# Performance work log

Measured on AMD Instinct MI355X. Metric: run time of the kernel, lower is better.

Reference implementation:

```python
import jax, jax.numpy as jnp
import numpy as np

E, TOPK, H, F, CAP, TP = 8, 2, 1024, 4096, 2048, 1
N = 8192  # tokens * topk (token copies)


def setup_inputs() -> dict:
    key = jax.random.key(0)
    ks = jax.random.split(key, 6)
    inputs_shard = jax.random.normal(ks[0], (N, H), jnp.float32)
    gate_weight = jax.random.uniform(ks[1], (N,), jnp.float32)
    choosed_experts = jax.random.randint(ks[2], (N,), 0, E, dtype=jnp.int32)
    new_index = jax.random.permutation(ks[3], N).astype(jnp.int32)
    w1 = jax.random.normal(ks[4], (E, F, H), jnp.float32) * 0.02
    w2 = jax.random.normal(ks[5], (E, H, F), jnp.float32) * 0.02
    return {"inputs_shard": inputs_shard, "gate_weight": gate_weight,
            "choosed_experts": choosed_experts, "new_index": new_index,
            "w1": w1, "w2": w2}


def _grouped_expert_mlp(x, experts, w1, w2):
    # capacity-based grouped GEMM: sort token copies by expert, pack into
    # (E, CAP, H), run batched fc1->gelu->fc2, unpack back to token order.
    n = x.shape[0]
    order = jnp.argsort(experts)                      # [N]
    se = experts[order]
    offsets = jnp.searchsorted(se, jnp.arange(E))     # start of each expert block
    rank = jnp.arange(n) - offsets[se]                # within-expert position
    valid = rank < CAP                                # CAP=2*N/E, ~never drops
    slot = jnp.where(valid, se * CAP + rank, E * CAP) # out-of-range -> dropped
    buf = jnp.zeros((E * CAP, x.shape[1]), x.dtype).at[slot].set(x[order], mode="drop")
    xe = buf.reshape(E, CAP, -1)                      # [E, CAP, H]
    h = jax.nn.gelu(jnp.einsum("ech,efh->ecf", xe, w1), approximate=False)
    ye = jnp.einsum("ecf,ehf->ech", h, w2).reshape(E * CAP, -1)
    y_sorted = jnp.where(valid[:, None], ye[jnp.clip(slot, 0, E * CAP - 1)], 0.0)
    return jnp.zeros_like(x).at[order].set(y_sorted)  # back to token-copy order


def reference(inputs_shard, gate_weight, choosed_experts, new_index, w1, w2):
    # expert compute, scaled by router probabilities (combine-side scaling)
    result = _grouped_expert_mlp(inputs_shard, choosed_experts, w1, w2)
    result = result * gate_weight[:, None]
    # scatter combine: output1[new_index] = result; full_output += output1
    full_output = jnp.zeros((N, H), result.dtype).at[new_index].set(result)
    # topk reduce: view(N//topk, topk, H).sum(1)
    topk_reduce = full_output.reshape(N // TOPK, TOPK, H).sum(1)
    # reduce_scatter over TP group; TP=1 => identity
    return topk_reduce
```

## Files before the change

kernel.cpp:

```cpp
#include <hip/hip_runtime.h>
#include <stdint.h>

#define N_TOK 8192
#define HDIM  1024
#define FDIM  4096
#define NEXP  8
#define MAXTILES 72
#define CVTZ  8
#define CVT1B 2048

typedef __attribute__((ext_vector_type(8))) __bf16 bf16x8;
typedef __attribute__((ext_vector_type(8))) unsigned short ushort8v;
typedef __attribute__((ext_vector_type(4))) unsigned short ushort4v;
typedef __attribute__((ext_vector_type(4))) float floatx4;

__device__ __forceinline__ unsigned short f2bf(float f) {
  union { float f; uint32_t u; } v; v.f = f;
  uint32_t u = v.u;
  return (unsigned short)((u + 0x7FFFu + ((u >> 16) & 1u)) >> 16);
}

__device__ __forceinline__ void load_lds16(const void* g, void* l) {
  __builtin_amdgcn_global_load_lds(
      (const __attribute__((address_space(1))) void*)(uintptr_t)g,
      (__attribute__((address_space(3))) void*)(uint32_t)(uintptr_t)l,
      16, 0, 0);
}


__global__ void k_count(const int* __restrict__ experts, int* __restrict__ meta) {
  int i = blockIdx.x * 256 + threadIdx.x;
  atomicAdd(&meta[experts[i]], 1);
}

__global__ void k_plan(int* __restrict__ meta) {
  if (threadIdx.x == 0) {
    int off = 0, nt = 0;
    for (int e = 0; e < NEXP; ++e) {
      int c = meta[e];
      meta[8 + e] = off;
      meta[16 + e] = off;
      int t = (c + 127) >> 7;
      for (int k = 0; k < t; ++k) meta[32 + nt++] = (e << 16) | k;
      off += c;
    }
    meta[24] = nt;
  }
}

__global__ void k_scatterpack(const float* __restrict__ x, const int* __restrict__ experts,
                              int* __restrict__ meta, int* __restrict__ order,
                              unsigned short* __restrict__ xs,
                              const float* __restrict__ w1, unsigned short* __restrict__ w1b) {
  int b = blockIdx.x;
  int t = threadIdx.x;
  if (b < N_TOK) {
    __shared__ int spos;
    if (t == 0) {
      int e = experts[b];
      int pos = atomicAdd(&meta[16 + e], 1);
      order[pos] = b;
      spos = pos;
    }
    __syncthreads();
    int s = spos;
    float4 v = *(const float4*)(x + (size_t)b * HDIM + t * 4);
    ushort4v u;
    u[0] = f2bf(v.x); u[1] = f2bf(v.y); u[2] = f2bf(v.z); u[3] = f2bf(v.w);
    *(ushort4v*)(xs + (size_t)s * HDIM + t * 4) = u;
  } else {
    int cb = b - N_TOK;
    const int per = (int)((size_t)NEXP * FDIM * HDIM / 4 / CVT1B);
    size_t base = (size_t)cb * per;
    for (int j = t; j < per; j += 256) {
      size_t idx = (base + j) * 4;
      float4 v = *(const float4*)(w1 + idx);
      ushort4v u;
      u[0] = f2bf(v.x); u[1] = f2bf(v.y); u[2] = f2bf(v.z); u[3] = f2bf(v.w);
      *(ushort4v*)(w1b + idx) = u;
    }
  }
}

template <bool PRE>
__global__ __launch_bounds__(256) void gemm1_t(
    const unsigned short* __restrict__ xs, const void* __restrict__ w1v,
    unsigned short* __restrict__ h1, const int* __restrict__ meta,
    const float* __restrict__ w2src, unsigned short* __restrict__ w2dst) {
  if constexpr (PRE) {
    if (blockIdx.z < CVTZ) {
      int cvtid = blockIdx.z * gridDim.x + blockIdx.x;
      const int per = (int)((size_t)NEXP * HDIM * FDIM / 4 / (CVTZ * (FDIM / 128)));
      size_t base = (size_t)cvtid * per;
      for (int j = threadIdx.x; j < per; j += 256) {
        size_t idx = (base + j) * 4;
        float4 v = *(const float4*)(w2src + idx);
        ushort4v u;
        u[0] = f2bf(v.x); u[1] = f2bf(v.y); u[2] = f2bf(v.z); u[3] = f2bf(v.w);
        *(ushort4v*)(w2dst + idx) = u;
      }
      return;
    }
  }
  __shared__ unsigned short As[2 * 128 * 32];
  __shared__ unsigned short Bs[2 * 128 * 32];

  int bx = blockIdx.z - (PRE ? CVTZ : 0);
  if (bx >= meta[24]) return;
  int entry = meta[32 + bx];
  int e = entry >> 16, mt = entry & 0xffff;
  int row0 = meta[8 + e] + mt * 128;
  int rend = meta[8 + e] + meta[e];
  int fBase = blockIdx.x * 128;

  int tid = threadIdx.x;
  int w = tid >> 6, lane = tid & 63;
  int r = lane & 15, q = lane >> 4;
  int wm = (w >> 1) * 64, wn = (w & 1) * 64;

  int ar0 = (w * 16) + (lane >> 2);
  int s0 = min(row0 + ar0, N_TOK - 1);
  int s1 = min(row0 + 64 + ar0, N_TOK - 1);
  const unsigned short* ag0 = xs + (size_t)s0 * HDIM + (lane & 3) * 8;
  const unsigned short* ag1 = xs + (size_t)s1 * HDIM + (lane & 3) * 8;
  unsigned short* al0 = &As[(w * 16) * 32];
  unsigned short* al1 = &As[(64 + w * 16) * 32];

  const unsigned short* bg0 = nullptr; const unsigned short* bg1 = nullptr;
  unsigned short* bl0 = nullptr; unsigned short* bl1 = nullptr;
  const float* wbase = nullptr; int brow = 0, bkk = 0;
  if constexpr (PRE) {
    const unsigned short* wb = (const unsigned short*)w1v;
    int br = w * 16 + (lane >> 2);
    bg0 = wb + ((size_t)e * FDIM + fBase + br) * HDIM + (lane & 3) * 8;
    bg1 = bg0 + (size_t)64 * HDIM;
    bl0 = &Bs[(w * 16) * 32];
    bl1 = &Bs[(64 + w * 16) * 32];
  } else {
    brow = tid >> 1; bkk = (tid & 1) * 16;
    wbase = (const float*)w1v + ((size_t)e * FDIM + fBase + brow) * HDIM + bkk;
  }

  auto stage = [&](int kk, int bo) {
    load_lds16(ag0 + kk, al0 + bo);
    load_lds16(ag1 + kk, al1 + bo);
    if constexpr (PRE) {
      load_lds16(bg0 + kk, bl0 + bo);
      load_lds16(bg1 + kk, bl1 + bo);
    } else {
      const float* gb = wbase + kk;
      float4 f0 = *(const float4*)(gb);
      float4 f1 = *(const float4*)(gb + 4);
      float4 f2 = *(const float4*)(gb + 8);
      float4 f3 = *(const float4*)(gb + 12);
      ushort8v u0, u1;
      u0[0] = f2bf(f0.x); u0[1] = f2bf(f0.y); u0[2] = f2bf(f0.z); u0[3] = f2bf(f0.w);
      u0[4] = f2bf(f1.x); u0[5] = f2bf(f1.y); u0[6] = f2bf(f1.z); u0[7] = f2bf(f1.w);
      u1[0] = f2bf(f2.x); u1[1] = f2bf(f2.y); u1[2] = f2bf(f2.z); u1[3] = f2bf(f2.w);
      u1[4] = f2bf(f3.x); u1[5] = f2bf(f3.y); u1[6] = f2bf(f3.z); u1[7] = f2bf(f3.w);
      *(ushort8v*)&Bs[bo + brow * 32 + bkk] = u0;
      *(ushort8v*)&Bs[bo + brow * 32 + bkk + 8] = u1;
    }
  };

  floatx4 acc[4][4];
#pragma unroll
  for (int i = 0; i < 4; ++i)
#pragma unroll
    for (int j = 0; j < 4; ++j) acc[i][j] = (floatx4){0.f, 0.f, 0.f, 0.f};

  stage(0, 0);
  for (int k0 = 0; k0 < HDIM; k0 += 32) {
    int bo = ((k0 >> 5) & 1) * 4096;
    __syncthreads();
    if (k0 + 32 < HDIM) stage(k0 + 32, bo ^ 4096);

    bf16x8 av[4], bv[4];
#pragma unroll
    for (int i = 0; i < 4; ++i)
      av[i] = __builtin_bit_cast(bf16x8, *(const ushort8v*)&As[bo + (wm + i * 16 + r) * 32 + q * 8]);
#pragma unroll
    for (int j = 0; j < 4; ++j)
      bv[j] = __builtin_bit_cast(bf16x8, *(const ushort8v*)&Bs[bo + (wn + j * 16 + r) * 32 + q * 8]);
#pragma unroll
    for (int i = 0; i < 4; ++i)
#pragma unroll
      for (int j = 0; j < 4; ++j)
        acc[i][j] = __builtin_amdgcn_mfma_f32_16x16x32_bf16(av[i], bv[j], acc[i][j], 0, 0, 0);
  }

#pragma unroll
  for (int i = 0; i < 4; ++i) {
    int mrow = row0 + wm + i * 16 + q * 4;
#pragma unroll
    for (int reg = 0; reg < 4; ++reg) {
      int s = mrow + reg;
      if (s < rend) {
        unsigned short* dst = h1 + (size_t)s * FDIM + fBase + wn + r;
#pragma unroll
        for (int j = 0; j < 4; ++j) {
          float v = acc[i][j][reg];
          float g = 0.5f * v * (1.0f + erff(v * 0.70710678118654752f));
          dst[j * 16] = f2bf(g);
        }
      }
    }
  }
}

template <bool PRE>
__global__ __launch_bounds__(256) void gemm2_t(
    const unsigned short* __restrict__ h1, const void* __restrict__ w2v,
    const float* __restrict__ gate, const int* __restrict__ new_index,
    float* __restrict__ out, const int* __restrict__ meta) {
  __shared__ unsigned short As[2 * 128 * 32];
  __shared__ unsigned short Bs[2 * 128 * 32];

  int bx = blockIdx.z;
  if (bx >= meta[24]) return;
  int entry = meta[32 + bx];
  int e = entry >> 16, mt = entry & 0xffff;
  int row0 = meta[8 + e] + mt * 128;
  int rend = meta[8 + e] + meta[e];
  int nBase = blockIdx.x * 128;
  int kStart = blockIdx.y * (FDIM / 2);
  int kEnd = kStart + (FDIM / 2);
  const int* order = meta + 256;

  int tid = threadIdx.x;
  int w = tid >> 6, lane = tid & 63;
  int r = lane & 15, q = lane >> 4;
  int wm = (w >> 1) * 64, wn = (w & 1) * 64;

  int ar0 = (w * 16) + (lane >> 2);
  int s0 = min(row0 + ar0, N_TOK - 1);
  int s1 = min(row0 + 64 + ar0, N_TOK - 1);
  const unsigned short* ag0 = h1 + (size_t)s0 * FDIM + (lane & 3) * 8;
  const unsigned short* ag1 = h1 + (size_t)s1 * FDIM + (lane & 3) * 8;
  unsigned short* al0 = &As[(w * 16) * 32];
  unsigned short* al1 = &As[(64 + w * 16) * 32];

  const unsigned short* bg0 = nullptr; const unsigned short* bg1 = nullptr;
  unsigned short* bl0 = nullptr; unsigned short* bl1 = nullptr;
  const float* wbase = nullptr; int brow = 0, bkk = 0;
  if constexpr (PRE) {
    const unsigned short* wb = (const unsigned short*)w2v;
    int br = w * 16 + (lane >> 2);
    bg0 = wb + ((size_t)e * HDIM + nBase + br) * FDIM + (lane & 3) * 8;
    bg1 = bg0 + (size_t)64 * FDIM;
    bl0 = &Bs[(w * 16) * 32];
    bl1 = &Bs[(64 + w * 16) * 32];
  } else {
    brow = tid >> 1; bkk = (tid & 1) * 16;
    wbase = (const float*)w2v + ((size_t)e * HDIM + nBase + brow) * FDIM + bkk;
  }

  auto stage = [&](int kk, int bo) {
    load_lds16(ag0 + kk, al0 + bo);
    load_lds16(ag1 + kk, al1 + bo);
    if constexpr (PRE) {
      load_lds16(bg0 + kk, bl0 + bo);
      load_lds16(bg1 + kk, bl1 + bo);
    } else {
      const float* gb = wbase + kk;
      float4 f0 = *(const float4*)(gb);
      float4 f1 = *(const float4*)(gb + 4);
      float4 f2 = *(const float4*)(gb + 8);
      float4 f3 = *(const float4*)(gb + 12);
      ushort8v u0, u1;
      u0[0] = f2bf(f0.x); u0[1] = f2bf(f0.y); u0[2] = f2bf(f0.z); u0[3] = f2bf(f0.w);
      u0[4] = f2bf(f1.x); u0[5] = f2bf(f1.y); u0[6] = f2bf(f1.z); u0[7] = f2bf(f1.w);
      u1[0] = f2bf(f2.x); u1[1] = f2bf(f2.y); u1[2] = f2bf(f2.z); u1[3] = f2bf(f2.w);
      u1[4] = f2bf(f3.x); u1[5] = f2bf(f3.y); u1[6] = f2bf(f3.z); u1[7] = f2bf(f3.w);
      *(ushort8v*)&Bs[bo + brow * 32 + bkk] = u0;
      *(ushort8v*)&Bs[bo + brow * 32 + bkk + 8] = u1;
    }
  };

  floatx4 acc[4][4];
#pragma unroll
  for (int i = 0; i < 4; ++i)
#pragma unroll
    for (int j = 0; j < 4; ++j) acc[i][j] = (floatx4){0.f, 0.f, 0.f, 0.f};

  stage(kStart, 0);
  for (int k0 = kStart; k0 < kEnd; k0 += 32) {
    int bo = (((k0 - kStart) >> 5) & 1) * 4096;
    __syncthreads();
    if (k0 + 32 < kEnd) stage(k0 + 32, bo ^ 4096);

    bf16x8 av[4], bv[4];
#pragma unroll
    for (int i = 0; i < 4; ++i)
      av[i] = __builtin_bit_cast(bf16x8, *(const ushort8v*)&As[bo + (wm + i * 16 + r) * 32 + q * 8]);
#pragma unroll
    for (int j = 0; j < 4; ++j)
      bv[j] = __builtin_bit_cast(bf16x8, *(const ushort8v*)&Bs[bo + (wn + j * 16 + r) * 32 + q * 8]);
#pragma unroll
    for (int i = 0; i < 4; ++i)
#pragma unroll
      for (int j = 0; j < 4; ++j)
        acc[i][j] = __builtin_amdgcn_mfma_f32_16x16x32_bf16(av[i], bv[j], acc[i][j], 0, 0, 0);
  }

#pragma unroll
  for (int i = 0; i < 4; ++i) {
    int mrow = row0 + wm + i * 16 + q * 4;
#pragma unroll
    for (int reg = 0; reg < 4; ++reg) {
      int s = mrow + reg;
      if (s < rend) {
        int itok = order[s];
        float gw = gate[itok];
        int jdx = new_index[itok];
        float* dst = out + (size_t)(jdx >> 1) * HDIM + nBase + wn + r;
#pragma unroll
        for (int j = 0; j < 4; ++j) atomicAdd(dst + j * 16, acc[i][j][reg] * gw);
      }
    }
  }
}

extern "C" void kernel_launch(void* const* d_in, const int* in_sizes, int n_in,
                              void* d_out, int out_size, void* d_ws, size_t ws_size,
                              hipStream_t stream) {
  const float* x        = (const float*)d_in[0];
  const float* gate     = (const float*)d_in[1];
  const int* experts    = (const int*)d_in[2];
  const int* new_index  = (const int*)d_in[3];
  const float* w1       = (const float*)d_in[4];
  const float* w2       = (const float*)d_in[5];
  float* out            = (float*)d_out;

  int* meta = (int*)d_ws;
  int* order = meta + 256;
  const size_t XS_OFF = 65536;
  const size_t XS_SZ  = (size_t)N_TOK * HDIM * 2;
  const size_t H1_SZ  = (size_t)N_TOK * FDIM * 2;
  const size_t W_SZ   = (size_t)NEXP * FDIM * HDIM * 2;
  unsigned short* xs  = (unsigned short*)((char*)d_ws + XS_OFF);
  unsigned short* h1  = (unsigned short*)((char*)d_ws + XS_OFF + XS_SZ);
  unsigned short* w1b = (unsigned short*)((char*)d_ws + XS_OFF + XS_SZ + H1_SZ);
  unsigned short* w2b = (unsigned short*)((char*)d_ws + XS_OFF + XS_SZ + H1_SZ + W_SZ);
  size_t need_small = XS_OFF + XS_SZ + H1_SZ;
  size_t need_big   = need_small + 2 * W_SZ;
  if (ws_size < need_small) return;
  bool big = ws_size >= need_big;

  hipMemsetAsync(d_ws, 0, 4096, stream);
  hipMemsetAsync(d_out, 0, (size_t)out_size * sizeof(float), stream);
  k_count<<<N_TOK / 256, 256, 0, stream>>>(experts, meta);
  k_plan<<<1, 64, 0, stream>>>(meta);
  k_scatterpack<<<N_TOK + (big ? CVT1B : 0), 256, 0, stream>>>(x, experts, meta, order, xs, w1, w1b);

  if (big) {
    gemm1_t<true><<<dim3(FDIM / 128, 1, MAXTILES + CVTZ), 256, 0, stream>>>(xs, w1b, h1, meta, w2, w2b);
    gemm2_t<true><<<dim3(HDIM / 128, 2, MAXTILES), 256, 0, stream>>>(h1, w2b, gate, new_index, out, meta);
  } else {
    gemm1_t<false><<<dim3(FDIM / 128, 1, MAXTILES), 256, 0, stream>>>(xs, w1, h1, meta, nullptr, nullptr);
    gemm2_t<false><<<dim3(HDIM / 128, 2, MAXTILES), 256, 0, stream>>>(h1, w2, gate, new_index, out, meta);
  }
}
```

Measured before the change: 728.8 us.

## Replace direct global-to-LDS loads with register-staged two-deep prefetch pipeline in GEMMs

Both grouped GEMM kernels drop the global_load_lds path and instead load tiles into registers two K-steps ahead, writing them to the alternate LDS buffer while the current buffer is consumed. The barrier is replaced by a custom waitcnt-on-lgkm plus s_barrier, which avoids waiting on outstanding global loads. Launch bounds gain a minimum of three blocks per CU to cap register use. The trade-off is extra VGPR pressure from holding two stage sets, plus redundant clamped loads at the tail.

```diff
diff --git a/kernel.cpp b/kernel.cpp
--- a/kernel.cpp
+++ b/kernel.cpp
@@ -8,23 +8,19 @@
 #define MAXTILES 72
 #define CVTZ  8
 #define CVT1B 2048
+#define BUFE  4096
 
 typedef __attribute__((ext_vector_type(8))) __bf16 bf16x8;
 typedef __attribute__((ext_vector_type(8))) unsigned short ushort8v;
 typedef __attribute__((ext_vector_type(4))) unsigned short ushort4v;
 typedef __attribute__((ext_vector_type(4))) float floatx4;
 
+#define BAR() asm volatile("s_waitcnt lgkmcnt(0)\ns_barrier" ::: "memory")
+
 __device__ __forceinline__ unsigned short f2bf(float f) {
   union { float f; uint32_t u; } v; v.f = f;
   uint32_t u = v.u;
   return (unsigned short)((u + 0x7FFFu + ((u >> 16) & 1u)) >> 16);
-}
-
-__device__ __forceinline__ void load_lds16(const void* g, void* l) {
-  __builtin_amdgcn_global_load_lds(
-      (const __attribute__((address_space(1))) void*)(uintptr_t)g,
-      (__attribute__((address_space(3))) void*)(uint32_t)(uintptr_t)l,
-      16, 0, 0);
 }
 
 
@@ -82,8 +78,14 @@
   }
 }
 
+struct StageSet {
+  uint4 a0, a1;
+  uint4 b0, b1;
+  float4 f0, f1, f2, f3;
+};
+
 template <bool PRE>
-__global__ __launch_bounds__(256) void gemm1_t(
+__global__ __launch_bounds__(256, 3) void gemm1_t(
     const unsigned short* __restrict__ xs, const void* __restrict__ w1v,
     unsigned short* __restrict__ h1, const int* __restrict__ meta,
     const float* __restrict__ w2src, unsigned short* __restrict__ w2dst) {
@@ -118,46 +120,50 @@
   int r = lane & 15, q = lane >> 4;
   int wm = (w >> 1) * 64, wn = (w & 1) * 64;
 
-  int ar0 = (w * 16) + (lane >> 2);
+  int ar0 = w * 16 + (lane >> 2);
+  int col8 = (lane & 3) * 8;
   int s0 = min(row0 + ar0, N_TOK - 1);
   int s1 = min(row0 + 64 + ar0, N_TOK - 1);
-  const unsigned short* ag0 = xs + (size_t)s0 * HDIM + (lane & 3) * 8;
-  const unsigned short* ag1 = xs + (size_t)s1 * HDIM + (lane & 3) * 8;
-  unsigned short* al0 = &As[(w * 16) * 32];
-  unsigned short* al1 = &As[(64 + w * 16) * 32];
-
-  const unsigned short* bg0 = nullptr; const unsigned short* bg1 = nullptr;
-  unsigned short* bl0 = nullptr; unsigned short* bl1 = nullptr;
+  const unsigned short* gA0 = xs + (size_t)s0 * HDIM + col8;
+  const unsigned short* gA1 = xs + (size_t)s1 * HDIM + col8;
+
+  const unsigned short* gB0 = nullptr; const unsigned short* gB1 = nullptr;
   const float* wbase = nullptr; int brow = 0, bkk = 0;
   if constexpr (PRE) {
     const unsigned short* wb = (const unsigned short*)w1v;
-    int br = w * 16 + (lane >> 2);
-    bg0 = wb + ((size_t)e * FDIM + fBase + br) * HDIM + (lane & 3) * 8;
-    bg1 = bg0 + (size_t)64 * HDIM;
-    bl0 = &Bs[(w * 16) * 32];
-    bl1 = &Bs[(64 + w * 16) * 32];
+    gB0 = wb + ((size_t)e * FDIM + fBase + ar0) * HDIM + col8;
+    gB1 = gB0 + (size_t)64 * HDIM;
   } else {
     brow = tid >> 1; bkk = (tid & 1) * 16;
     wbase = (const float*)w1v + ((size_t)e * FDIM + fBase + brow) * HDIM + bkk;
   }
 
-  auto stage = [&](int kk, int bo) {
-    load_lds16(ag0 + kk, al0 + bo);
-    load_lds16(ag1 + kk, al1 + bo);
+  auto load_set = [&](StageSet& s, int kk) {
+    s.a0 = *(const uint4*)(gA0 + kk);
+    s.a1 = *(const uint4*)(gA1 + kk);
     if constexpr (PRE) {
-      load_lds16(bg0 + kk, bl0 + bo);
-      load_lds16(bg1 + kk, bl1 + bo);
+      s.b0 = *(const uint4*)(gB0 + kk);
+      s.b1 = *(const uint4*)(gB1 + kk);
     } else {
       const float* gb = wbase + kk;
-      float4 f0 = *(const float4*)(gb);
-      float4 f1 = *(const float4*)(gb + 4);
-      float4 f2 = *(const float4*)(gb + 8);
-      float4 f3 = *(const float4*)(gb + 12);
+      s.f0 = *(const float4*)(gb);
+      s.f1 = *(const float4*)(gb + 4);
+      s.f2 = *(const float4*)(gb + 8);
+      s.f3 = *(const float4*)(gb + 12);
+    }
+  };
+  auto write_set = [&](const StageSet& s, int bo) {
+    *(uint4*)&As[bo + ar0 * 32 + col8] = s.a0;
+    *(uint4*)&As[bo + (64 + ar0) * 32 + col8] = s.a1;
+    if constexpr (PRE) {
+      *(uint4*)&Bs[bo + ar0 * 32 + col8] = s.b0;
+      *(uint4*)&Bs[bo + (64 + ar0) * 32 + col8] = s.b1;
+    } else {
       ushort8v u0, u1;
-      u0[0] = f2bf(f0.x); u0[1] = f2bf(f0.y); u0[2] = f2bf(f0.z); u0[3] = f2bf(f0.w);
-      u0[4] = f2bf(f1.x); u0[5] = f2bf(f1.y); u0[6] = f2bf(f1.z); u0[7] = f2bf(f1.w);
-      u1[0] = f2bf(f2.x); u1[1] = f2bf(f2.y); u1[2] = f2bf(f2.z); u1[3] = f2bf(f2.w);
-      u1[4] = f2bf(f3.x); u1[5] = f2bf(f3.y); u1[6] = f2bf(f3.z); u1[7] = f2bf(f3.w);
+      u0[0] = f2bf(s.f0.x); u0[1] = f2bf(s.f0.y); u0[2] = f2bf(s.f0.z); u0[3] = f2bf(s.f0.w);
+      u0[4] = f2bf(s.f1.x); u0[5] = f2bf(s.f1.y); u0[6] = f2bf(s.f1.z); u0[7] = f2bf(s.f1.w);
+      u1[0] = f2bf(s.f2.x); u1[1] = f2bf(s.f2.y); u1[2] = f2bf(s.f2.z); u1[3] = f2bf(s.f2.w);
+      u1[4] = f2bf(s.f3.x); u1[5] = f2bf(s.f3.y); u1[6] = f2bf(s.f3.z); u1[7] = f2bf(s.f3.w);
       *(ushort8v*)&Bs[bo + brow * 32 + bkk] = u0;
       *(ushort8v*)&Bs[bo + brow * 32 + bkk + 8] = u1;
     }
@@ -169,12 +175,7 @@
 #pragma unroll
     for (int j = 0; j < 4; ++j) acc[i][j] = (floatx4){0.f, 0.f, 0.f, 0.f};
 
-  stage(0, 0);
-  for (int k0 = 0; k0 < HDIM; k0 += 32) {
-    int bo = ((k0 >> 5) & 1) * 4096;
-    __syncthreads();
-    if (k0 + 32 < HDIM) stage(k0 + 32, bo ^ 4096);
-
+  auto compute = [&](int bo) {
     bf16x8 av[4], bv[4];
 #pragma unroll
     for (int i = 0; i < 4; ++i)
@@ -187,6 +188,25 @@
 #pragma unroll
       for (int j = 0; j < 4; ++j)
         acc[i][j] = __builtin_amdgcn_mfma_f32_16x16x32_bf16(av[i], bv[j], acc[i][j], 0, 0, 0);
+  };
+
+  StageSet st0, st1;
+  load_set(st0, 0);
+  load_set(st1, 32);
+  write_set(st0, 0);
+  load_set(st0, 64);
+  BAR();
+  for (int k0 = 0; k0 < HDIM; k0 += 64) {
+    compute(0);
+    write_set(st1, BUFE);
+    load_set(st1, min(k0 + 96, HDIM - 32));
+    BAR();
+    compute(BUFE);
+    if (k0 + 64 < HDIM) {
+      write_set(st0, 0);
+      load_set(st0, min(k0 + 128, HDIM - 32));
+      BAR();
+    }
   }
 
 #pragma unroll
@@ -209,7 +229,7 @@
 }
 
 template <bool PRE>
-__global__ __launch_bounds__(256) void gemm2_t(
+__global__ __launch_bounds__(256, 3) void gemm2_t(
     const unsigned short* __restrict__ h1, const void* __restrict__ w2v,
     const float* __restrict__ gate, const int* __restrict__ new_index,
     float* __restrict__ out, const int* __restrict__ meta) {
@@ -232,46 +252,50 @@
   int r = lane & 15, q = lane >> 4;
   int wm = (w >> 1) * 64, wn = (w & 1) * 64;
 
-  int ar0 = (w * 16) + (lane >> 2);
+  int ar0 = w * 16 + (lane >> 2);
+  int col8 = (lane & 3) * 8;
   int s0 = min(row0 + ar0, N_TOK - 1);
   int s1 = min(row0 + 64 + ar0, N_TOK - 1);
-  const unsigned short* ag0 = h1 + (size_t)s0 * FDIM + (lane & 3) * 8;
-  const unsigned short* ag1 = h1 + (size_t)s1 * FDIM + (lane & 3) * 8;
-  unsigned short* al0 = &As[(w * 16) * 32];
-  unsigned short* al1 = &As[(64 + w * 16) * 32];
-
-  const unsigned short* bg0 = nullptr; const unsigned short* bg1 = nullptr;
-  unsigned short* bl0 = nullptr; unsigned short* bl1 = nullptr;
+  const unsigned short* gA0 = h1 + (size_t)s0 * FDIM + col8;
+  const unsigned short* gA1 = h1 + (size_t)s1 * FDIM + col8;
+
+  const unsigned short* gB0 = nullptr; const unsigned short* gB1 = nullptr;
   const float* wbase = nullptr; int brow = 0, bkk = 0;
   if constexpr (PRE) {
     const unsigned short* wb = (const unsigned short*)w2v;
-    int br = w * 16 + (lane >> 2);
-    bg0 = wb + ((size_t)e * HDIM + nBase + br) * FDIM + (lane & 3) * 8;
-    bg1 = bg0 + (size_t)64 * FDIM;
-    bl0 = &Bs[(w * 16) * 32];
-    bl1 = &Bs[(64 + w * 16) * 32];
+    gB0 = wb + ((size_t)e * HDIM + nBase + ar0) * FDIM + col8;
+    gB1 = gB0 + (size_t)64 * FDIM;
   } else {
     brow = tid >> 1; bkk = (tid & 1) * 16;
     wbase = (const float*)w2v + ((size_t)e * HDIM + nBase + brow) * FDIM + bkk;
   }
 
-  auto stage = [&](int kk, int bo) {
-    load_lds16(ag0 + kk, al0 + bo);
-    load_lds16(ag1 + kk, al1 + bo);
+  auto load_set = [&](StageSet& s, int kk) {
+    s.a0 = *(const uint4*)(gA0 + kk);
+    s.a1 = *(const uint4*)(gA1 + kk);
     if constexpr (PRE) {
-      load_lds16(bg0 + kk, bl0 + bo);
-      load_lds16(bg1 + kk, bl1 + bo);
+      s.b0 = *(const uint4*)(gB0 + kk);
+      s.b1 = *(const uint4*)(gB1 + kk);
     } else {
       const float* gb = wbase + kk;
-      float4 f0 = *(const float4*)(gb);
-      float4 f1 = *(const float4*)(gb + 4);
-      float4 f2 = *(const float4*)(gb + 8);
-      float4 f3 = *(const float4*)(gb + 12);
+      s.f0 = *(const float4*)(gb);
+      s.f1 = *(const float4*)(gb + 4);
+      s.f2 = *(const float4*)(gb + 8);
+      s.f3 = *(const float4*)(gb + 12);
+    }
+  };
+  auto write_set = [&](const StageSet& s, int bo) {
+    *(uint4*)&As[bo + ar0 * 32 + col8] = s.a0;
+    *(uint4*)&As[bo + (64 + ar0) * 32 + col8] = s.a1;
+    if constexpr (PRE) {
+      *(uint4*)&Bs[bo + ar0 * 32 + col8] = s.b0;
+      *(uint4*)&Bs[bo + (64 + ar0) * 32 + col8] = s.b1;
+    } else {
       ushort8v u0, u1;
-      u0[0] = f2bf(f0.x); u0[1] = f2bf(f0.y); u0[2] = f2bf(f0.z); u0[3] = f2bf(f0.w);
-      u0[4] = f2bf(f1.x); u0[5] = f2bf(f1.y); u0[6] = f2bf(f1.z); u0[7] = f2bf(f1.w);
-      u1[0] = f2bf(f2.x); u1[1] = f2bf(f2.y); u1[2] = f2bf(f2.z); u1[3] = f2bf(f2.w);
-      u1[4] = f2bf(f3.x); u1[5] = f2bf(f3.y); u1[6] = f2bf(f3.z); u1[7] = f2bf(f3.w);
+      u0[0] = f2bf(s.f0.x); u0[1] = f2bf(s.f0.y); u0[2] = f2bf(s.f0.z); u0[3] = f2bf(s.f0.w);
+      u0[4] = f2bf(s.f1.x); u0[5] = f2bf(s.f1.y); u0[6] = f2bf(s.f1.z); u0[7] = f2bf(s.f1.w);
+      u1[0] = f2bf(s.f2.x); u1[1] = f2bf(s.f2.y); u1[2] = f2bf(s.f2.z); u1[3] = f2bf(s.f2.w);
+      u1[4] = f2bf(s.f3.x); u1[5] = f2bf(s.f3.y); u1[6] = f2bf(s.f3.z); u1[7] = f2bf(s.f3.w);
       *(ushort8v*)&Bs[bo + brow * 32 + bkk] = u0;
       *(ushort8v*)&Bs[bo + brow * 32 + bkk + 8] = u1;
     }
@@ -283,12 +307,7 @@
 #pragma unroll
     for (int j = 0; j < 4; ++j) acc[i][j] = (floatx4){0.f, 0.f, 0.f, 0.f};
 
-  stage(kStart, 0);
-  for (int k0 = kStart; k0 < kEnd; k0 += 32) {
-    int bo = (((k0 - kStart) >> 5) & 1) * 4096;
-    __syncthreads();
-    if (k0 + 32 < kEnd) stage(k0 + 32, bo ^ 4096);
-
+  auto compute = [&](int bo) {
     bf16x8 av[4], bv[4];
 #pragma unroll
     for (int i = 0; i < 4; ++i)
@@ -301,6 +320,25 @@
 #pragma unroll
       for (int j = 0; j < 4; ++j)
         acc[i][j] = __builtin_amdgcn_mfma_f32_16x16x32_bf16(av[i], bv[j], acc[i][j], 0, 0, 0);
+  };
+
+  StageSet st0, st1;
+  load_set(st0, kStart);
+  load_set(st1, kStart + 32);
+  write_set(st0, 0);
+  load_set(st0, kStart + 64);
+  BAR();
+  for (int k0 = kStart; k0 < kEnd; k0 += 64) {
+    compute(0);
+    write_set(st1, BUFE);
+    load_set(st1, min(k0 + 96, kEnd - 32));
+    BAR();
+    compute(BUFE);
+    if (k0 + 64 < kEnd) {
+      write_set(st0, 0);
+      load_set(st0, min(k0 + 128, kEnd - 32));
+      BAR();
+    }
   }
 
 #pragma unroll
```

After: 1.466 ms. 101% more time.
